# Performance work log

Hardware: AMD Instinct MI355X
Metric: run time of the kernel (lower is better)

## Reference

```python
import jax, jax.numpy as jnp
import numpy as np

B, T = 4, 512
V, D, L, H, F = 32000, 1024, 12, 16, 4096
HD = D // H
CUTS = [0, 2000, 8000, V]
SHRINK = 4


def layer_norm(x, s, b, eps=1e-5):
    m = jnp.mean(x, axis=-1, keepdims=True)
    v = jnp.var(x, axis=-1, keepdims=True)
    return (x - m) * jax.lax.rsqrt(v + eps) * s + b


def rel_shift(x):
    # Transformer-XL relative shift. x: [B, H, T, S] with S == T.
    b, h, t, s = x.shape
    x = jnp.pad(x, ((0, 0), (0, 0), (0, 0), (1, 0)))
    x = x.reshape(b, h, s + 1, t)[:, :, 1:, :]
    return x.reshape(b, h, t, s)


def sinusoid_pos_emb(seq_len, dim):
    # positions seq_len-1 ... 0 (TXL convention), [seq_len, dim]
    pos = jnp.arange(seq_len - 1, -1, -1.0, dtype=jnp.float32)
    inv_freq = 1.0 / (10000.0 ** (jnp.arange(0, dim, 2, dtype=jnp.float32) / dim))
    ang = pos[:, None] * inv_freq[None, :]
    return jnp.concatenate([jnp.sin(ang), jnp.cos(ang)], axis=-1)


def setup_inputs() -> dict:
    key = jax.random.key(0)
    ks = iter(jax.random.split(key, 64))

    def n(shape, std=0.02):
        return jax.random.normal(next(ks), shape, dtype=jnp.float32) * std

    hids = [D // (SHRINK ** i) for i in range(3)]  # 1024, 256, 64
    inp = {}
    inp['x'] = jax.random.randint(next(ks), (B, T), 0, V)
    inp['emb_0'] = n([CUTS[1] - CUTS[0], hids[0]])
    inp['emb_1'] = n([CUTS[2] - CUTS[1], hids[1]])
    inp['emb_2'] = n([CUTS[3] - CUTS[2], hids[2]])
    inp['proj_1'] = n([hids[1], D], 0.01)
    inp['proj_2'] = n([hids[2], D], 0.01)
    inp['out_bias'] = jnp.zeros([V], jnp.float32)
    inp['r_w_bias'] = n([1, 1, H, HD])
    inp['r_r_bias'] = n([1, 1, H, HD])
    inp['ln1_s'] = jnp.ones([L, D], jnp.float32)
    inp['ln1_b'] = jnp.zeros([L, D], jnp.float32)
    inp['Wq'] = n([L, D, D]); inp['bq'] = jnp.zeros([L, D], jnp.float32)
    inp['Wk'] = n([L, D, D]); inp['bk'] = jnp.zeros([L, D], jnp.float32)
    inp['Wv'] = n([L, D, D]); inp['bv'] = jnp.zeros([L, D], jnp.float32)
    inp['Wr'] = n([L, D, D])  # relative position projection (no bias)
    inp['Wo'] = n([L, D, D]); inp['bo'] = jnp.zeros([L, D], jnp.float32)
    inp['ln2_s'] = jnp.ones([L, D], jnp.float32)
    inp['ln2_b'] = jnp.zeros([L, D], jnp.float32)
    inp['W1'] = n([L, D, F]); inp['b1'] = jnp.zeros([L, F], jnp.float32)
    inp['W2'] = n([L, F, D]); inp['b2'] = jnp.zeros([L, D], jnp.float32)
    return inp


def forward(x, emb_0, emb_1, emb_2, proj_1, proj_2, out_bias, r_w_bias, r_r_bias,
            ln1_s, ln1_b, Wq, bq, Wk, bk, Wv, bv, Wr, Wo, bo, ln2_s, ln2_b,
            W1, b1, W2, b2):
    Bx, Tx = x.shape
    # --- adaptive input embedding (clustered table + up-projection, scaled) ---
    embs = [emb_0, emb_1, emb_2]
    projs = [None, proj_1, proj_2]
    h = jnp.zeros((Bx, Tx, D), jnp.float32)
    for i in range(3):
        lo, hi = CUTS[i], CUTS[i + 1]
        in_bucket = (x >= lo) & (x < hi)
        idx = jnp.clip(x - lo, 0, hi - lo - 1)
        e = embs[i][idx]  # [B, T, hid_i]
        if projs[i] is not None:
            e = e @ projs[i]  # -> [B, T, D]
        h = h + jnp.where(in_bucket[..., None], e, 0.0)
    h = h * jnp.sqrt(jnp.float32(D))

    pemb = sinusoid_pos_emb(Tx, D)                  # [T, D]
    causal = jnp.tril(jnp.ones((Tx, Tx), bool))     # [T, T]
    scale = 1.0 / np.sqrt(HD)

    for i in range(L):
        # --- TXL relative-position multi-head attention (pre-norm) ---
        a_in = layer_norm(h, ln1_s[i], ln1_b[i])
        q = (a_in @ Wq[i] + bq[i]).reshape(Bx, Tx, H, HD)
        k = (a_in @ Wk[i] + bk[i]).reshape(Bx, Tx, H, HD)
        v = (a_in @ Wv[i] + bv[i]).reshape(Bx, Tx, H, HD)
        r_k = (pemb @ Wr[i]).reshape(Tx, H, HD)     # [T, H, HD]
        content = jnp.einsum('bthd,bshd->bhts', q + r_w_bias[0, 0], k)
        rel = jnp.einsum('bthd,shd->bhts', q + r_r_bias[0, 0], r_k)
        logits = (content + rel_shift(rel)) * scale
        logits = jnp.where(causal[None, None], logits, jnp.float32(-1e30))
        attn = jax.nn.softmax(logits, axis=-1)
        o = jnp.einsum('bhts,bshd->bthd', attn, v).reshape(Bx, Tx, D)
        h = h + (o @ Wo[i] + bo[i])
        # --- FFN (pre-norm, GELU) ---
        f_in = layer_norm(h, ln2_s[i], ln2_b[i])
        h = h + (jax.nn.gelu(f_in @ W1[i] + b1[i]) @ W2[i] + b2[i])

    # --- tied adaptive-softmax output projection ---
    W_full = jnp.concatenate([emb_0, emb_1 @ proj_1, emb_2 @ proj_2], axis=0)  # [V, D]
    return h @ W_full.T + out_bias  # [B, T, V]


def reference(x, emb_0, emb_1, emb_2, proj_1, proj_2, out_bias, r_w_bias, r_r_bias,
              ln1_s, ln1_b, Wq, bq, Wk, bk, Wv, bv, Wr, Wo, bo, ln2_s, ln2_b,
              W1, b1, W2, b2):
    return forward(x, emb_0, emb_1, emb_2, proj_1, proj_2, out_bias, r_w_bias,
                   r_r_bias, ln1_s, ln1_b, Wq, bq, Wk, bk, Wv, bv, Wr, Wo, bo,
                   ln2_s, ln2_b, W1, b1, W2, b2)
```

## Files before the change

kernel.cpp:

```cpp
#include <hip/hip_runtime.h>

using us = unsigned short;
typedef short short8v __attribute__((ext_vector_type(8)));
typedef float float4v __attribute__((ext_vector_type(4)));

constexpr int NB  = 4;
constexpr int NT  = 512;
constexpr int ND  = 1024;
constexpr int NL  = 12;
constexpr int NH  = 16;
constexpr int NF  = 4096;
constexpr int NHD = 64;
constexpr int NBT = NB * NT;
constexpr int NV  = 32000;
constexpr long QOFF = (long)NBT * ND;
constexpr long RKL  = 640L * 1024;

__device__ __forceinline__ us f2bf(float f) {
    unsigned u = __float_as_uint(f);
    u += 0x7fffu + ((u >> 16) & 1u);
    return (us)(u >> 16);
}

__device__ __forceinline__ void gload16(const us* g, us* l) {
    __builtin_amdgcn_global_load_lds(
        (const __attribute__((address_space(1))) void*)g,
        (__attribute__((address_space(3))) void*)l, 16, 0, 0);
}

template<int BM, int BN, int EPI, bool OUTBF>
__global__ __launch_bounds__(256)
void bgemm_k(const us* __restrict__ A, const us* __restrict__ B, void* Cv,
             const float* __restrict__ bias, const float* addsrc,
             const float* __restrict__ p0, const float* __restrict__ p1,
             us* __restrict__ vtp,
             int N, int K, int lda, int ldb, int ldc,
             int bdiv, long sAb, long sAh, long sBb, long sBh, long sCb, long sCh)
{
    constexpr int BK  = 64;
    constexpr int WTM = BM / 2, WTN = BN / 2;
    constexpr int FM  = WTM / 16, FN = WTN / 16;
    constexpr int AI  = BM / 32;
    constexpr int BI  = BN / 32;
    static_assert(BM % 32 == 0 && BN % 32 == 0, "");

    long coff = 0;
    if (bdiv > 0) {
        int z = blockIdx.z, zb = z / bdiv, zh = z % bdiv;
        A += zb * sAb + zh * sAh;
        B += zb * sBb + zh * sBh;
        coff = zb * sCb + zh * sCh;
    }
    float* Cf = (float*)Cv + coff;
    us*    Ch = (us*)Cv + coff;
    if (addsrc) addsrc += coff;

    __shared__ __align__(16) us As[2 * BM * BK];
    __shared__ __align__(16) us Bs[2 * BN * BK];

    const int tid  = threadIdx.x;
    const int lane = tid & 63;
    const int w    = tid >> 6;
    const int wm   = w >> 1;
    const int wn   = w & 1;
    const int row0 = blockIdx.y * BM;
    const int col0 = blockIdx.x * BN;

    float4v acc[FM][FN];
#pragma unroll
    for (int i = 0; i < FM; ++i)
#pragma unroll
        for (int j = 0; j < FN; ++j) acc[i][j] = (float4v)0.f;

    auto stage = [&](int buf, int k0) {
        us* Ad = As + buf * (BM * BK);
        us* Bd = Bs + buf * (BN * BK);
#pragma unroll
        for (int i = 0; i < AI; ++i) {
            int rb = w * (BM / 4) + i * 8;
            int r  = rb + (lane >> 3);
            int sc8 = ((lane & 7) ^ (r & 7)) << 3;
            gload16(A + (long)(row0 + r) * lda + k0 + sc8, Ad + rb * 64);
        }
#pragma unroll
        for (int i = 0; i < BI; ++i) {
            int rb = w * (BN / 4) + i * 8;
            int r  = rb + (lane >> 3);
            int sc8 = ((lane & 7) ^ (r & 7)) << 3;
            gload16(B + (long)(col0 + r) * ldb + k0 + sc8, Bd + rb * 64);
        }
    };

    stage(0, 0);
    __syncthreads();
    int cur = 0;
    for (int k0 = 0; k0 < K; k0 += BK) {
        if (k0 + BK < K) stage(cur ^ 1, k0 + BK);
        const char* Ac = (const char*)(As + cur * (BM * BK));
        const char* Bc = (const char*)(Bs + cur * (BN * BK));
#pragma unroll
        for (int ks = 0; ks < 2; ++ks) {
            short8v af[FM], bfr[FN];
            int sw = ks * 4 + (lane >> 4);
#pragma unroll
            for (int i = 0; i < FM; ++i) {
                int r = wm * WTM + i * 16 + (lane & 15);
                af[i] = *reinterpret_cast<const short8v*>(Ac + r * 128 + ((sw ^ (r & 7)) << 4));
            }
#pragma unroll
            for (int j = 0; j < FN; ++j) {
                int r = wn * WTN + j * 16 + (lane & 15);
                bfr[j] = *reinterpret_cast<const short8v*>(Bc + r * 128 + ((sw ^ (r & 7)) << 4));
            }
#pragma unroll
            for (int i = 0; i < FM; ++i)
#pragma unroll
                for (int j = 0; j < FN; ++j)
                    acc[i][j] = __builtin_amdgcn_mfma_f32_16x16x32_bf16(af[i], bfr[j], acc[i][j], 0, 0, 0);
        }
        __syncthreads();
        cur ^= 1;
    }

#pragma unroll
    for (int i = 0; i < FM; ++i) {
        int growb = row0 + wm * WTM + i * 16 + ((lane >> 4) << 2);
#pragma unroll
        for (int j = 0; j < FN; ++j) {
            int gcol = col0 + wn * WTN + j * 16 + (lane & 15);
            if (EPI == 3) {
                int seg = gcol >> 10, c = gcol & 1023;
                float bb = bias[gcol];
                if (seg == 2) {
                    unsigned lo = (unsigned)f2bf(acc[i][j][0] + bb)
                                | ((unsigned)f2bf(acc[i][j][1] + bb) << 16);
                    unsigned hi = (unsigned)f2bf(acc[i][j][2] + bb)
                                | ((unsigned)f2bf(acc[i][j][3] + bb) << 16);
                    int bidx = growb >> 9, tb = growb & 511;
                    uint2 pk; pk.x = lo; pk.y = hi;
                    *reinterpret_cast<uint2*>(
                        vtp + ((long)((bidx * 16 + (c >> 6)) * 64 + (c & 63)) << 9) + tb) = pk;
                } else {
                    us* base = (us*)Cv;
#pragma unroll
                    for (int r = 0; r < 4; ++r) {
                        int gr = growb + r;
                        float v = acc[i][j][r] + bb;
                        long o = (long)gr * 1024 + c;
                        if (seg == 0) {
                            base[o]        = f2bf(v + p0[c]);
                            base[o + QOFF] = f2bf(v + p1[c]);
                        } else base[o + 2 * QOFF] = f2bf(v);
                    }
                }
            } else {
                if (gcol >= N) continue;
#pragma unroll
                for (int r = 0; r < 4; ++r) {
                    int gr = growb + r;
                    float v = acc[i][j][r];
                    if (bias) v += bias[gcol];
                    if (EPI == 1) {
                        float xx = v;
                        v = 0.5f * xx * (1.f + tanhf(0.7978845608028654f
                                                     * (xx + 0.044715f * xx * xx * xx)));
                    }
                    if (addsrc) v += addsrc[(long)gr * ldc + gcol];
                    if (OUTBF) Ch[(long)gr * ldc + gcol] = f2bf(v);
                    else       Cf[(long)gr * ldc + gcol] = v;
                }
            }
        }
    }
}

__global__ __launch_bounds__(256)
void ffnred_k(const float* __restrict__ part, const float* __restrict__ b2v,
              float* __restrict__ h)
{
    long i = ((long)blockIdx.x * 256 + threadIdx.x) * 4;
    float4 a0 = *reinterpret_cast<const float4*>(part + i);
    float4 a1 = *reinterpret_cast<const float4*>(part + i + 2097152);
    float4 a2 = *reinterpret_cast<const float4*>(part + i + 4194304);
    float4 a3 = *reinterpret_cast<const float4*>(part + i + 6291456);
    float4 hv = *reinterpret_cast<const float4*>(h + i);
    float4 bb = *reinterpret_cast<const float4*>(b2v + (int)(i & 1023));
    hv.x += a0.x + a1.x + a2.x + a3.x + bb.x;
    hv.y += a0.y + a1.y + a2.y + a3.y + bb.y;
    hv.z += a0.z + a1.z + a2.z + a3.z + bb.z;
    hv.w += a0.w + a1.w + a2.w + a3.w + bb.w;
    *reinterpret_cast<float4*>(h + i) = hv;
}

__global__ __launch_bounds__(256)
void fattn_k(const us* __restrict__ qkv, const us* __restrict__ vt,
             const us* __restrict__ rk, us* __restrict__ obuf)
{
    __shared__ __align__(16) us lds_k[64 * 64];
    __shared__ __align__(16) us lds_v[64 * 64];
    __shared__ __align__(16) us lds_rk[64 * 64];
    __shared__ __align__(16) us lds_p[4 * 16 * 64];
    __shared__ float lds_r[4 * 16 * 132];

    const int tid = threadIdx.x, lane = tid & 63, w = tid >> 6;
    const int qt = blockIdx.x, bh = blockIdx.y;
    const int b = bh >> 4, h = bh & 15;
    const int t0 = qt * 64;
    const int rg = lane >> 4, lc = lane & 15;

    const us* qwb = qkv + ((long)b * 512) * 1024 + h * 64;
    const us* qrb = qwb + QOFF;
    const us* kb  = qwb + 2 * QOFF;
    const us* vtb = vt + (long)bh * 64 * 512;
    const us* rkb = rk + h * 64;

    short8v aqw[2], aqr[2];
    {
        long qrow = (long)(t0 + w * 16 + lc) * 1024;
        int ko = rg * 8;
        aqw[0] = *(const short8v*)(qwb + qrow + ko);
        aqw[1] = *(const short8v*)(qwb + qrow + 32 + ko);
        aqr[0] = *(const short8v*)(qrb + qrow + ko);
        aqr[1] = *(const short8v*)(qrb + qrow + 32 + ko);
    }

    float4v oacc[4];
#pragma unroll
    for (int i = 0; i < 4; ++i) oacc[i] = (float4v)0.f;
    float mrow[4] = {-3e38f, -3e38f, -3e38f, -3e38f};
    float lrow[4] = {0.f, 0.f, 0.f, 0.f};

    float* rbase = lds_r + w * (16 * 132);
    us*    pbase = lds_p + w * (16 * 64);

    auto stage_rk = [&](int j0) {
#pragma unroll
        for (int i = 0; i < 2; ++i) {
            int rb = w * 16 + i * 8;
            int r  = rb + (lane >> 3);
            int sl = ((lane & 7) ^ (r & 7)) << 3;
            gload16(rkb + (long)(j0 + r) * 1024 + sl, lds_rk + rb * 64);
        }
    };
    auto rel_half = [&](int wbase) {
#pragma unroll
        for (int jn = 0; jn < 4; ++jn) {
            float4v rf = (float4v)0.f;
#pragma unroll
            for (int kk = 0; kk < 2; ++kk) {
                int r = jn * 16 + lc;
                int sw = kk * 4 + rg;
                short8v bf = *(const short8v*)((const char*)lds_rk + r * 128 + ((sw ^ (r & 7)) << 4));
                rf = __builtin_amdgcn_mfma_f32_16x16x32_bf16(aqr[kk], bf, rf, 0, 0, 0);
            }
#pragma unroll
            for (int pr = 0; pr < 4; ++pr)
                rbase[(rg * 4 + pr) * 132 + wbase + jn * 16 + lc] = rf[pr];
        }
    };

    const int nst = qt + 1;
    for (int st = 0; st < nst; ++st) {
        const int s0 = st * 64;
        const int jb = (st - qt) * 64 + 448;
        const int sb = ((st - qt + 7) & 1) << 6;

#pragma unroll
        for (int i = 0; i < 2; ++i) {
            int rb = w * 16 + i * 8;
            int r  = rb + (lane >> 3);
            int sl = ((lane & 7) ^ (r & 7)) << 3;
            gload16(kb + (long)(s0 + r) * 1024 + sl, lds_k + rb * 64);
            gload16(vtb + (long)r * 512 + s0 + sl, lds_v + rb * 64);
        }
        if (st == 0) {
            stage_rk(jb);
            __syncthreads();
            rel_half(sb);
            __syncthreads();
            stage_rk(jb + 64);
            __syncthreads();
        } else {
            stage_rk(jb + 64);
            __syncthreads();
        }

        float4v sfr[4];
#pragma unroll
        for (int sn = 0; sn < 4; ++sn) {
            sfr[sn] = (float4v)0.f;
#pragma unroll
            for (int kk = 0; kk < 2; ++kk) {
                int r = sn * 16 + lc;
                int sw = kk * 4 + rg;
                short8v bf = *(const short8v*)((const char*)lds_k + r * 128 + ((sw ^ (r & 7)) << 4));
                sfr[sn] = __builtin_amdgcn_mfma_f32_16x16x32_bf16(aqw[kk], bf, sfr[sn], 0, 0, 0);
            }
        }
        rel_half(sb ^ 64);

        float pv[4][4];
        float rmax[4] = {-3e38f, -3e38f, -3e38f, -3e38f};
#pragma unroll
        for (int pr = 0; pr < 4; ++pr) {
            int tt = rg * 4 + pr;
            int tw = w * 16 + tt;
#pragma unroll
            for (int sn = 0; sn < 4; ++sn) {
                int ss = sn * 16 + lc;
                int slot = (sb + ss + 63 - tw) & 127;
                float lg = (sfr[sn][pr] + rbase[tt * 132 + slot]) * 0.125f;
                if (ss > t0 - s0 + tw) lg = -1e30f;
                pv[sn][pr] = lg;
                rmax[pr] = fmaxf(rmax[pr], lg);
            }
        }
#pragma unroll
        for (int o = 1; o < 16; o <<= 1)
#pragma unroll
            for (int pr = 0; pr < 4; ++pr)
                rmax[pr] = fmaxf(rmax[pr], __shfl_xor(rmax[pr], o));
        float rsum[4];
#pragma unroll
        for (int pr = 0; pr < 4; ++pr) {
            float mn = fmaxf(mrow[pr], rmax[pr]);
            float al = __expf(mrow[pr] - mn);
            mrow[pr] = mn;
            lrow[pr] *= al;
            float s = 0.f;
#pragma unroll
            for (int sn = 0; sn < 4; ++sn) {
                float p = __expf(pv[sn][pr] - mn);
                pv[sn][pr] = p;
                s += p;
            }
            rsum[pr] = s;
#pragma unroll
            for (int dn = 0; dn < 4; ++dn) oacc[dn][pr] *= al;
        }
#pragma unroll
        for (int o = 1; o < 16; o <<= 1)
#pragma unroll
            for (int pr = 0; pr < 4; ++pr)
                rsum[pr] += __shfl_xor(rsum[pr], o);
#pragma unroll
        for (int pr = 0; pr < 4; ++pr) lrow[pr] += rsum[pr];

#pragma unroll
        for (int pr = 0; pr < 4; ++pr) {
            int row = rg * 4 + pr;
#pragma unroll
            for (int sn = 0; sn < 4; ++sn) {
                int col = sn * 16 + lc;
                *(us*)((char*)pbase + row * 128 + (((col >> 3) ^ (row & 7)) << 4) + (col & 7) * 2)
                    = f2bf(pv[sn][pr]);
            }
        }
        short8v pa[2];
#pragma unroll
        for (int kk = 0; kk < 2; ++kk)
            pa[kk] = *(const short8v*)((const char*)pbase + lc * 128 + (((kk * 4 + rg) ^ (lc & 7)) << 4));
#pragma unroll
        for (int dn = 0; dn < 4; ++dn) {
#pragma unroll
            for (int kk = 0; kk < 2; ++kk) {
                int r = dn * 16 + lc;
                int sw = kk * 4 + rg;
                short8v vb = *(const short8v*)((const char*)lds_v + r * 128 + ((sw ^ (r & 7)) << 4));
                oacc[dn] = __builtin_amdgcn_mfma_f32_16x16x32_bf16(pa[kk], vb, oacc[dn], 0, 0, 0);
            }
        }
        __syncthreads();
    }
#pragma unroll
    for (int pr = 0; pr < 4; ++pr) {
        int t = t0 + w * 16 + rg * 4 + pr;
        float inv = 1.f / lrow[pr];
        long rowo = ((long)b * 512 + t) * 1024 + h * 64;
#pragma unroll
        for (int dn = 0; dn < 4; ++dn)
            obuf[rowo + dn * 16 + lc] = f2bf(oacc[dn][pr] * inv);
    }
}

__global__ __launch_bounds__(256)
void tconv_k(const float* __restrict__ in, us* __restrict__ out, int R, int C,
             long inL, long outL)
{
    in  += (long)blockIdx.z * inL;
    out += (long)blockIdx.z * outL;
    __shared__ float t[32][33];
    int c0 = blockIdx.x * 32, r0 = blockIdx.y * 32;
    int tx = threadIdx.x & 31, ty = threadIdx.x >> 5;
#pragma unroll
    for (int j = 0; j < 4; ++j)
        t[ty + j * 8][tx] = in[(long)(r0 + ty + j * 8) * C + c0 + tx];
    __syncthreads();
#pragma unroll
    for (int j = 0; j < 4; ++j)
        out[(long)(c0 + ty + j * 8) * R + r0 + tx] = f2bf(t[tx][ty + j * 8]);
}

__global__ __launch_bounds__(256)
void conv_k(const float* __restrict__ in, us* __restrict__ out, long n)
{
    long i = ((long)blockIdx.x * 256 + threadIdx.x) * 4;
    if (i >= n) return;
    float4 v = *reinterpret_cast<const float4*>(in + i);
    uint2 p;
    p.x = (unsigned)f2bf(v.x) | ((unsigned)f2bf(v.y) << 16);
    p.y = (unsigned)f2bf(v.z) | ((unsigned)f2bf(v.w) << 16);
    *reinterpret_cast<uint2*>(out + i) = p;
}

__global__ __launch_bounds__(256)
void rkpad12_k(us* __restrict__ rk)
{
    int i = blockIdx.x * 256 + threadIdx.x;
    int l = i >> 13, r = i & 8191;
    reinterpret_cast<uint4*>(rk + (long)l * RKL + 512 * 1024)[r] = make_uint4(0, 0, 0, 0);
}

__global__ __launch_bounds__(256)
void bcat_k(const float* __restrict__ bq, const float* __restrict__ bk,
            const float* __restrict__ bv, float* __restrict__ o)
{
    int i = blockIdx.x * 256 + threadIdx.x;
    int l = i / 3072, rr = i % 3072, seg = rr >> 10, c = rr & 1023;
    const float* s = seg == 0 ? bq : seg == 1 ? bk : bv;
    o[i] = s[l * 1024 + c];
}

__global__ __launch_bounds__(256)
void ln_k(const float* __restrict__ x, us* __restrict__ y,
          const float* __restrict__ sc, const float* __restrict__ bi)
{
    int row = blockIdx.x;
    const float* xr = x + (long)row * ND;
    int d4 = threadIdx.x * 4;
    float4 v = *reinterpret_cast<const float4*>(&xr[d4]);
    float sum = v.x + v.y + v.z + v.w;
    float sq  = v.x * v.x + v.y * v.y + v.z * v.z + v.w * v.w;
#pragma unroll
    for (int o = 32; o; o >>= 1) { sum += __shfl_xor(sum, o); sq += __shfl_xor(sq, o); }
    __shared__ float red[8];
    int w = threadIdx.x >> 6;
    if ((threadIdx.x & 63) == 0) { red[w] = sum; red[4 + w] = sq; }
    __syncthreads();
    sum = red[0] + red[1] + red[2] + red[3];
    sq  = red[4] + red[5] + red[6] + red[7];
    float mean = sum * (1.f / ND);
    float var  = fmaxf(sq * (1.f / ND) - mean * mean, 0.f);
    float inv  = rsqrtf(var + 1e-5f);
    float4 s4 = *reinterpret_cast<const float4*>(&sc[d4]);
    float4 b4 = *reinterpret_cast<const float4*>(&bi[d4]);
    uint2 p;
    p.x = (unsigned)f2bf((v.x - mean) * inv * s4.x + b4.x)
        | ((unsigned)f2bf((v.y - mean) * inv * s4.y + b4.y) << 16);
    p.y = (unsigned)f2bf((v.z - mean) * inv * s4.z + b4.z)
        | ((unsigned)f2bf((v.w - mean) * inv * s4.w + b4.w) << 16);
    *reinterpret_cast<uint2*>(y + (long)row * ND + d4) = p;
}

__global__ __launch_bounds__(256)
void pemb_k(us* __restrict__ p)
{
    int t = blockIdx.x;
    float pos = (float)(NT - 1 - t);
    for (int j = threadIdx.x; j < ND / 2; j += 256) {
        float invf = expf(-(float)j * (9.210340371976184f / 512.0f));
        float ang  = pos * invf;
        p[(long)t * ND + j]           = f2bf(sinf(ang));
        p[(long)t * ND + ND / 2 + j]  = f2bf(cosf(ang));
    }
}

__global__ __launch_bounds__(256)
void embed_k(const int* __restrict__ x,
             const float* __restrict__ e0, const float* __restrict__ e1,
             const float* __restrict__ e2, const float* __restrict__ p1,
             const float* __restrict__ p2, float* __restrict__ h)
{
    __shared__ float e[256];
    int tok = blockIdx.x;
    int v = x[tok];
    float* outp = h + (long)tok * ND;
    if (v < 2000) {
        const float* r = e0 + (long)v * ND;
        for (int d = threadIdx.x; d < ND; d += 256) outp[d] = r[d] * 32.0f;
    } else if (v < 8000) {
        const float* r = e1 + (long)(v - 2000) * 256;
        e[threadIdx.x] = r[threadIdx.x];
        __syncthreads();
        for (int d = threadIdx.x; d < ND; d += 256) {
            float acc = 0.f;
#pragma unroll 4
            for (int i = 0; i < 256; ++i) acc += e[i] * p1[(long)i * ND + d];
            outp[d] = acc * 32.0f;
        }
    } else {
        const float* r = e2 + (long)(v - 8000) * 64;
        if (threadIdx.x < 64) e[threadIdx.x] = r[threadIdx.x];
        __syncthreads();
        for (int d = threadIdx.x; d < ND; d += 256) {
            float acc = 0.f;
#pragma unroll 4
            for (int i = 0; i < 64; ++i) acc += e[i] * p2[(long)i * ND + d];
            outp[d] = acc * 32.0f;
        }
    }
}

extern "C" void kernel_launch(void* const* d_in, const int* in_sizes, int n_in,
                              void* d_out, int out_size, void* d_ws, size_t ws_size,
                              hipStream_t stream)
{
    (void)in_sizes; (void)n_in; (void)out_size;
    const int*   x     = (const int*)  d_in[0];
    const float* emb0  = (const float*)d_in[1];
    const float* emb1  = (const float*)d_in[2];
    const float* emb2  = (const float*)d_in[3];
    const float* proj1 = (const float*)d_in[4];
    const float* proj2 = (const float*)d_in[5];
    const float* obias = (const float*)d_in[6];
    const float* rwb   = (const float*)d_in[7];
    const float* rrb   = (const float*)d_in[8];
    const float* ln1s  = (const float*)d_in[9];
    const float* ln1b  = (const float*)d_in[10];
    const float* Wq    = (const float*)d_in[11];
    const float* bq    = (const float*)d_in[12];
    const float* Wk    = (const float*)d_in[13];
    const float* bk    = (const float*)d_in[14];
    const float* Wv    = (const float*)d_in[15];
    const float* bv    = (const float*)d_in[16];
    const float* Wr    = (const float*)d_in[17];
    const float* Wo    = (const float*)d_in[18];
    const float* bo    = (const float*)d_in[19];
    const float* ln2s  = (const float*)d_in[20];
    const float* ln2b  = (const float*)d_in[21];
    const float* W1    = (const float*)d_in[22];
    const float* b1    = (const float*)d_in[23];
    const float* W2    = (const float*)d_in[24];
    const float* b2    = (const float*)d_in[25];
    float* out = (float*)d_out;

    us* ob      = (us*)out;
    us* qkvbuf  = ob;
    us* mid_bf  = ob +  6291456;
    us* vt_bf   = ob + 14680064;
    us* o_bf    = ob + 16777216;
    us* ain_bf  = ob + 18874368;
    us* rk_all  = ob + 20971520;
    us* pemb_bf = ob + 28835840;
    us* wqkv_sc = ob + 29360128;
    us* wr_sc   = ob + 32505856;
    us* wo_sc   = ob + 33554432;
    us* w1_sc   = ob + 34603008;
    us* w2_sc   = ob + 38797312;
    float* pffn = out + 21495808;

    float* wsf      = (float*)d_ws;
    float* h        = wsf;
    us*    h_bf     = (us*)(wsf + 2097152);
    us*    hp1_bf   = h_bf   + 2097152;
    us*    hp2_bf   = hp1_bf + 524288;
    us*    emb0_bf  = hp2_bf + 131072;
    us*    emb1_bf  = emb0_bf + 2097152;
    us*    emb2_bf  = emb1_bf + 1572864;
    us*    proj1_bf = emb2_bf + 1540096;
    us*    proj2_bf = proj1_bf + 262144;
    float* bqkv     = (float*)(proj2_bf + 65536);
    us*    wqkv_all = (us*)(bqkv + 36864);
    us*    wr_all   = wqkv_all + (long)NL * 3072 * 1024;
    us*    wo_all   = wr_all   + (long)NL * 1024 * 1024;
    us*    w1_all   = wo_all   + (long)NL * 1024 * 1024;
    us*    w2_all   = w1_all   + (long)NL * 4096 * 1024;
    const bool big  = ws_size >= (size_t)352273408;

    bcat_k<<<144, 256, 0, stream>>>(bq, bk, bv, bqkv);
    conv_k<<<2000, 256, 0, stream>>>(emb0,  emb0_bf,  2048000);
    conv_k<<<1500, 256, 0, stream>>>(emb1,  emb1_bf,  1536000);
    conv_k<<<1500, 256, 0, stream>>>(emb2,  emb2_bf,  1536000);
    conv_k<<<256,  256, 0, stream>>>(proj1, proj1_bf, 262144);
    conv_k<<<64,   256, 0, stream>>>(proj2, proj2_bf, 65536);
    pemb_k<<<NT, 256, 0, stream>>>(pemb_bf);
    rkpad12_k<<<384, 256, 0, stream>>>(rk_all);
    embed_k<<<NBT, 256, 0, stream>>>(x, emb0, emb1, emb2, proj1, proj2, h);
    if (big) {
        tconv_k<<<dim3(32, 32, NL), 256, 0, stream>>>(Wq, wqkv_all,           1024, 1024, 1048576, 3145728);
        tconv_k<<<dim3(32, 32, NL), 256, 0, stream>>>(Wk, wqkv_all + 1048576, 1024, 1024, 1048576, 3145728);
        tconv_k<<<dim3(32, 32, NL), 256, 0, stream>>>(Wv, wqkv_all + 2097152, 1024, 1024, 1048576, 3145728);
        tconv_k<<<dim3(32, 32, NL), 256, 0, stream>>>(Wr, wr_all, 1024, 1024, 1048576, 1048576);
        tconv_k<<<dim3(32, 32, NL), 256, 0, stream>>>(Wo, wo_all, 1024, 1024, 1048576, 1048576);
        tconv_k<<<dim3(128, 32, NL), 256, 0, stream>>>(W1, w1_all, 1024, 4096, 4194304, 4194304);
        tconv_k<<<dim3(32, 128, NL), 256, 0, stream>>>(W2, w2_all, 4096, 1024, 4194304, 4194304);
        bgemm_k<64, 64, 0, true><<<dim3(16, 8, NL), 256, 0, stream>>>(
            pemb_bf, wr_all, rk_all, nullptr, nullptr, nullptr, nullptr, nullptr,
            1024, 1024, 1024, 1024, 1024,
            1, 0, 0, 1048576, 0, RKL, 0);
    }

    for (int l = 0; l < NL; ++l) {
        const us* wqkv_t = big ? wqkv_all + (long)l * 3145728 : wqkv_sc;
        const us* wo_t   = big ? wo_all   + (long)l * 1048576 : wo_sc;
        const us* w1_t   = big ? w1_all   + (long)l * 4194304 : w1_sc;
        const us* w2_t   = big ? w2_all   + (long)l * 4194304 : w2_sc;
        if (!big) {
            const long wOff = (long)l * ND * ND;
            tconv_k<<<dim3(32, 32), 256, 0, stream>>>(Wq + wOff, wqkv_sc,           1024, 1024, 0, 0);
            tconv_k<<<dim3(32, 32), 256, 0, stream>>>(Wk + wOff, wqkv_sc + 1048576, 1024, 1024, 0, 0);
            tconv_k<<<dim3(32, 32), 256, 0, stream>>>(Wv + wOff, wqkv_sc + 2097152, 1024, 1024, 0, 0);
            tconv_k<<<dim3(32, 32), 256, 0, stream>>>(Wr + wOff, wr_sc, 1024, 1024, 0, 0);
            tconv_k<<<dim3(32, 32), 256, 0, stream>>>(Wo + wOff, wo_sc, 1024, 1024, 0, 0);
            tconv_k<<<dim3(128, 32), 256, 0, stream>>>(W1 + (long)l * ND * NF, w1_sc, 1024, 4096, 0, 0);
            tconv_k<<<dim3(32, 128), 256, 0, stream>>>(W2 + (long)l * ND * NF, w2_sc, 4096, 1024, 0, 0);
            bgemm_k<64, 64, 0, true><<<dim3(16, 8, 1), 256, 0, stream>>>(
                pemb_bf, wr_sc, rk_all + (long)l * RKL, nullptr, nullptr, nullptr, nullptr, nullptr,
                1024, 1024, 1024, 1024, 1024, 0, 0, 0, 0, 0, 0, 0);
        }

        ln_k<<<NBT, 256, 0, stream>>>(h, ain_bf, ln1s + l * ND, ln1b + l * ND);
        bgemm_k<128, 64, 3, true><<<dim3(48, 16, 1), 256, 0, stream>>>(
            ain_bf, wqkv_t, qkvbuf, bqkv + l * 3072, nullptr, rwb, rrb, vt_bf,
            3072, 1024, 1024, 1024, 1024, 0, 0, 0, 0, 0, 0, 0);
        fattn_k<<<dim3(8, NB * NH), 256, 0, stream>>>(
            qkvbuf, vt_bf, rk_all + (long)l * RKL, o_bf);
        bgemm_k<64, 64, 0, false><<<dim3(16, 32, 1), 256, 0, stream>>>(
            o_bf, wo_t, h, bo + l * ND, h, nullptr, nullptr, nullptr,
            1024, 1024, 1024, 1024, 1024, 0, 0, 0, 0, 0, 0, 0);

        ln_k<<<NBT, 256, 0, stream>>>(h, ain_bf, ln2s + l * ND, ln2b + l * ND);
        bgemm_k<128, 128, 1, true><<<dim3(32, 16, 1), 256, 0, stream>>>(
            ain_bf, w1_t, mid_bf, b1 + (long)l * NF, nullptr, nullptr, nullptr, nullptr,
            4096, 1024, 1024, 1024, 4096, 0, 0, 0, 0, 0, 0, 0);
        bgemm_k<128, 128, 0, false><<<dim3(8, 16, 4), 256, 0, stream>>>(
            mid_bf, w2_t, pffn, nullptr, nullptr, nullptr, nullptr, nullptr,
            1024, 1024, 4096, 4096, 1024,
            1, 1024, 0, 1024, 0, 2097152, 0);
        ffnred_k<<<2048, 256, 0, stream>>>(pffn, b2 + (long)l * ND, h);
    }

    conv_k<<<2048, 256, 0, stream>>>(h, h_bf, (long)NBT * ND);
    bgemm_k<128, 64, 0, false><<<dim3(32, 16, 1), 256, 0, stream>>>(
        h_bf, emb0_bf, out, obias, nullptr, nullptr, nullptr, nullptr,
        2000, 1024, 1024, 1024, NV, 0, 0, 0, 0, 0, 0, 0);
    bgemm_k<64, 64, 0, true><<<dim3(4, 32, 1), 256, 0, stream>>>(
        h_bf, proj1_bf, hp1_bf, nullptr, nullptr, nullptr, nullptr, nullptr,
        256, 1024, 1024, 1024, 256, 0, 0, 0, 0, 0, 0, 0);
    bgemm_k<128, 128, 0, false><<<dim3(47, 16, 1), 256, 0, stream>>>(
        hp1_bf, emb1_bf, out + 2000, obias + 2000, nullptr, nullptr, nullptr, nullptr,
        6000, 256, 256, 256, NV, 0, 0, 0, 0, 0, 0, 0);
    bgemm_k<64, 64, 0, true><<<dim3(1, 32, 1), 256, 0, stream>>>(
        h_bf, proj2_bf, hp2_bf, nullptr, nullptr, nullptr, nullptr, nullptr,
        64, 1024, 1024, 1024, 64, 0, 0, 0, 0, 0, 0, 0);
    bgemm_k<128, 128, 0, false><<<dim3(188, 16, 1), 256, 0, stream>>>(
        hp2_bf, emb2_bf, out + 8000, obias + 8000, nullptr, nullptr, nullptr, nullptr,
        24000, 64, 64, 64, NV, 0, 0, 0, 0, 0, 0, 0);
}
```

Before: 2.572 ms.

## Fuse residual reductions with layernorm, split-K Wo GEMM, pair attention query tiles

```diff
diff --git a/kernel.cpp b/kernel.cpp
--- a/kernel.cpp
+++ b/kernel.cpp
@@ -174,22 +174,52 @@
     }
 }
 
-__global__ __launch_bounds__(256)
-void ffnred_k(const float* __restrict__ part, const float* __restrict__ b2v,
-              float* __restrict__ h)
-{
-    long i = ((long)blockIdx.x * 256 + threadIdx.x) * 4;
-    float4 a0 = *reinterpret_cast<const float4*>(part + i);
-    float4 a1 = *reinterpret_cast<const float4*>(part + i + 2097152);
-    float4 a2 = *reinterpret_cast<const float4*>(part + i + 4194304);
-    float4 a3 = *reinterpret_cast<const float4*>(part + i + 6291456);
+template<int NPART, int MODE>
+__global__ __launch_bounds__(256)
+void redln_k(const float* __restrict__ part, const float* __restrict__ bias,
+             float* __restrict__ h, us* __restrict__ outb,
+             const float* __restrict__ sc, const float* __restrict__ bi)
+{
+    int row = blockIdx.x;
+    int d4 = threadIdx.x * 4;
+    long i = (long)row * ND + d4;
     float4 hv = *reinterpret_cast<const float4*>(h + i);
-    float4 bb = *reinterpret_cast<const float4*>(b2v + (int)(i & 1023));
-    hv.x += a0.x + a1.x + a2.x + a3.x + bb.x;
-    hv.y += a0.y + a1.y + a2.y + a3.y + bb.y;
-    hv.z += a0.z + a1.z + a2.z + a3.z + bb.z;
-    hv.w += a0.w + a1.w + a2.w + a3.w + bb.w;
+    float4 bb = *reinterpret_cast<const float4*>(bias + d4);
+    hv.x += bb.x; hv.y += bb.y; hv.z += bb.z; hv.w += bb.w;
+#pragma unroll
+    for (int z = 0; z < NPART; ++z) {
+        float4 a = *reinterpret_cast<const float4*>(part + (long)z * 2097152 + i);
+        hv.x += a.x; hv.y += a.y; hv.z += a.z; hv.w += a.w;
+    }
     *reinterpret_cast<float4*>(h + i) = hv;
+    if (MODE == 1) {
+        uint2 p;
+        p.x = (unsigned)f2bf(hv.x) | ((unsigned)f2bf(hv.y) << 16);
+        p.y = (unsigned)f2bf(hv.z) | ((unsigned)f2bf(hv.w) << 16);
+        *reinterpret_cast<uint2*>(outb + i) = p;
+    } else {
+        float sum = hv.x + hv.y + hv.z + hv.w;
+        float sq  = hv.x * hv.x + hv.y * hv.y + hv.z * hv.z + hv.w * hv.w;
+#pragma unroll
+        for (int o = 32; o; o >>= 1) { sum += __shfl_xor(sum, o); sq += __shfl_xor(sq, o); }
+        __shared__ float red[8];
+        int w = threadIdx.x >> 6;
+        if ((threadIdx.x & 63) == 0) { red[w] = sum; red[4 + w] = sq; }
+        __syncthreads();
+        sum = red[0] + red[1] + red[2] + red[3];
+        sq  = red[4] + red[5] + red[6] + red[7];
+        float mean = sum * (1.f / ND);
+        float var  = fmaxf(sq * (1.f / ND) - mean * mean, 0.f);
+        float inv  = rsqrtf(var + 1e-5f);
+        float4 s4 = *reinterpret_cast<const float4*>(&sc[d4]);
+        float4 b4 = *reinterpret_cast<const float4*>(&bi[d4]);
+        uint2 p;
+        p.x = (unsigned)f2bf((hv.x - mean) * inv * s4.x + b4.x)
+            | ((unsigned)f2bf((hv.y - mean) * inv * s4.y + b4.y) << 16);
+        p.y = (unsigned)f2bf((hv.z - mean) * inv * s4.z + b4.z)
+            | ((unsigned)f2bf((hv.w - mean) * inv * s4.w + b4.w) << 16);
+        *reinterpret_cast<uint2*>(outb + i) = p;
+    }
 }
 
 __global__ __launch_bounds__(256)
@@ -203,9 +233,8 @@
     __shared__ float lds_r[4 * 16 * 132];
 
     const int tid = threadIdx.x, lane = tid & 63, w = tid >> 6;
-    const int qt = blockIdx.x, bh = blockIdx.y;
+    const int qtp = blockIdx.x, bh = blockIdx.y;
     const int b = bh >> 4, h = bh & 15;
-    const int t0 = qt * 64;
     const int rg = lane >> 4, lc = lane & 15;
 
     const us* qwb = qkv + ((long)b * 512) * 1024 + h * 64;
@@ -214,172 +243,177 @@
     const us* vtb = vt + (long)bh * 64 * 512;
     const us* rkb = rk + h * 64;
 
-    short8v aqw[2], aqr[2];
-    {
-        long qrow = (long)(t0 + w * 16 + lc) * 1024;
-        int ko = rg * 8;
-        aqw[0] = *(const short8v*)(qwb + qrow + ko);
-        aqw[1] = *(const short8v*)(qwb + qrow + 32 + ko);
-        aqr[0] = *(const short8v*)(qrb + qrow + ko);
-        aqr[1] = *(const short8v*)(qrb + qrow + 32 + ko);
-    }
-
-    float4v oacc[4];
-#pragma unroll
-    for (int i = 0; i < 4; ++i) oacc[i] = (float4v)0.f;
-    float mrow[4] = {-3e38f, -3e38f, -3e38f, -3e38f};
-    float lrow[4] = {0.f, 0.f, 0.f, 0.f};
-
     float* rbase = lds_r + w * (16 * 132);
     us*    pbase = lds_p + w * (16 * 64);
 
-    auto stage_rk = [&](int j0) {
-#pragma unroll
-        for (int i = 0; i < 2; ++i) {
-            int rb = w * 16 + i * 8;
-            int r  = rb + (lane >> 3);
-            int sl = ((lane & 7) ^ (r & 7)) << 3;
-            gload16(rkb + (long)(j0 + r) * 1024 + sl, lds_rk + rb * 64);
-        }
-    };
-    auto rel_half = [&](int wbase) {
-#pragma unroll
-        for (int jn = 0; jn < 4; ++jn) {
-            float4v rf = (float4v)0.f;
-#pragma unroll
-            for (int kk = 0; kk < 2; ++kk) {
-                int r = jn * 16 + lc;
-                int sw = kk * 4 + rg;
-                short8v bf = *(const short8v*)((const char*)lds_rk + r * 128 + ((sw ^ (r & 7)) << 4));
-                rf = __builtin_amdgcn_mfma_f32_16x16x32_bf16(aqr[kk], bf, rf, 0, 0, 0);
-            }
-#pragma unroll
-            for (int pr = 0; pr < 4; ++pr)
-                rbase[(rg * 4 + pr) * 132 + wbase + jn * 16 + lc] = rf[pr];
-        }
-    };
-
-    const int nst = qt + 1;
-    for (int st = 0; st < nst; ++st) {
-        const int s0 = st * 64;
-        const int jb = (st - qt) * 64 + 448;
-        const int sb = ((st - qt + 7) & 1) << 6;
-
-#pragma unroll
-        for (int i = 0; i < 2; ++i) {
-            int rb = w * 16 + i * 8;
-            int r  = rb + (lane >> 3);
-            int sl = ((lane & 7) ^ (r & 7)) << 3;
-            gload16(kb + (long)(s0 + r) * 1024 + sl, lds_k + rb * 64);
-            gload16(vtb + (long)r * 512 + s0 + sl, lds_v + rb * 64);
-        }
-        if (st == 0) {
-            stage_rk(jb);
+    for (int hh = 0; hh < 2; ++hh) {
+        const int qt = hh ? 7 - qtp : qtp;
+        const int t0 = qt * 64;
+
+        short8v aqw[2], aqr[2];
+        {
+            long qrow = (long)(t0 + w * 16 + lc) * 1024;
+            int ko = rg * 8;
+            aqw[0] = *(const short8v*)(qwb + qrow + ko);
+            aqw[1] = *(const short8v*)(qwb + qrow + 32 + ko);
+            aqr[0] = *(const short8v*)(qrb + qrow + ko);
+            aqr[1] = *(const short8v*)(qrb + qrow + 32 + ko);
+        }
+
+        float4v oacc[4];
+#pragma unroll
+        for (int i = 0; i < 4; ++i) oacc[i] = (float4v)0.f;
+        float mrow[4] = {-3e38f, -3e38f, -3e38f, -3e38f};
+        float lrow[4] = {0.f, 0.f, 0.f, 0.f};
+
+        auto stage_rk = [&](int j0) {
+#pragma unroll
+            for (int i = 0; i < 2; ++i) {
+                int rb = w * 16 + i * 8;
+                int r  = rb + (lane >> 3);
+                int sl = ((lane & 7) ^ (r & 7)) << 3;
+                gload16(rkb + (long)(j0 + r) * 1024 + sl, lds_rk + rb * 64);
+            }
+        };
+        auto rel_half = [&](int wbase) {
+#pragma unroll
+            for (int jn = 0; jn < 4; ++jn) {
+                float4v rf = (float4v)0.f;
+#pragma unroll
+                for (int kk = 0; kk < 2; ++kk) {
+                    int r = jn * 16 + lc;
+                    int sw = kk * 4 + rg;
+                    short8v bf = *(const short8v*)((const char*)lds_rk + r * 128 + ((sw ^ (r & 7)) << 4));
+                    rf = __builtin_amdgcn_mfma_f32_16x16x32_bf16(aqr[kk], bf, rf, 0, 0, 0);
+                }
+#pragma unroll
+                for (int pr = 0; pr < 4; ++pr)
+                    rbase[(rg * 4 + pr) * 132 + wbase + jn * 16 + lc] = rf[pr];
+            }
+        };
+
+        const int nst = qt + 1;
+        for (int st = 0; st < nst; ++st) {
+            const int s0 = st * 64;
+            const int jb = (st - qt) * 64 + 448;
+            const int sb = ((st - qt + 7) & 1) << 6;
+
+#pragma unroll
+            for (int i = 0; i < 2; ++i) {
+                int rb = w * 16 + i * 8;
+                int r  = rb + (lane >> 3);
+                int sl = ((lane & 7) ^ (r & 7)) << 3;
+                gload16(kb + (long)(s0 + r) * 1024 + sl, lds_k + rb * 64);
+                gload16(vtb + (long)r * 512 + s0 + sl, lds_v + rb * 64);
+            }
+            if (st == 0) {
+                stage_rk(jb);
+                __syncthreads();
+                rel_half(sb);
+                __syncthreads();
+                stage_rk(jb + 64);
+                __syncthreads();
+            } else {
+                stage_rk(jb + 64);
+                __syncthreads();
+            }
+
+            float4v sfr[4];
+#pragma unroll
+            for (int sn = 0; sn < 4; ++sn) {
+                sfr[sn] = (float4v)0.f;
+#pragma unroll
+                for (int kk = 0; kk < 2; ++kk) {
+                    int r = sn * 16 + lc;
+                    int sw = kk * 4 + rg;
+                    short8v bf = *(const short8v*)((const char*)lds_k + r * 128 + ((sw ^ (r & 7)) << 4));
+                    sfr[sn] = __builtin_amdgcn_mfma_f32_16x16x32_bf16(aqw[kk], bf, sfr[sn], 0, 0, 0);
+                }
+            }
+            rel_half(sb ^ 64);
+
+            float pv[4][4];
+            float rmax[4] = {-3e38f, -3e38f, -3e38f, -3e38f};
+#pragma unroll
+            for (int pr = 0; pr < 4; ++pr) {
+                int tt = rg * 4 + pr;
+                int tw = w * 16 + tt;
+#pragma unroll
+                for (int sn = 0; sn < 4; ++sn) {
+                    int ss = sn * 16 + lc;
+                    int slot = (sb + ss + 63 - tw) & 127;
+                    float lg = (sfr[sn][pr] + rbase[tt * 132 + slot]) * 0.125f;
+                    if (ss > t0 - s0 + tw) lg = -1e30f;
+                    pv[sn][pr] = lg;
+                    rmax[pr] = fmaxf(rmax[pr], lg);
+                }
+            }
+#pragma unroll
+            for (int o = 1; o < 16; o <<= 1)
+#pragma unroll
+                for (int pr = 0; pr < 4; ++pr)
+                    rmax[pr] = fmaxf(rmax[pr], __shfl_xor(rmax[pr], o));
+            float rsum[4];
+#pragma unroll
+            for (int pr = 0; pr < 4; ++pr) {
+                float mn = fmaxf(mrow[pr], rmax[pr]);
+                float al = __expf(mrow[pr] - mn);
+                mrow[pr] = mn;
+                lrow[pr] *= al;
+                float s = 0.f;
+#pragma unroll
+                for (int sn = 0; sn < 4; ++sn) {
+                    float p = __expf(pv[sn][pr] - mn);
+                    pv[sn][pr] = p;
+                    s += p;
+                }
+                rsum[pr] = s;
+#pragma unroll
+                for (int dn = 0; dn < 4; ++dn) oacc[dn][pr] *= al;
+            }
+#pragma unroll
+            for (int o = 1; o < 16; o <<= 1)
+#pragma unroll
+                for (int pr = 0; pr < 4; ++pr)
+                    rsum[pr] += __shfl_xor(rsum[pr], o);
+#pragma unroll
+            for (int pr = 0; pr < 4; ++pr) lrow[pr] += rsum[pr];
+
+#pragma unroll
+            for (int pr = 0; pr < 4; ++pr) {
+                int row = rg * 4 + pr;
+#pragma unroll
+                for (int sn = 0; sn < 4; ++sn) {
+                    int col = sn * 16 + lc;
+                    *(us*)((char*)pbase + row * 128 + (((col >> 3) ^ (row & 7)) << 4) + (col & 7) * 2)
+                        = f2bf(pv[sn][pr]);
+                }
+            }
+            short8v pa[2];
+#pragma unroll
+            for (int kk = 0; kk < 2; ++kk)
+                pa[kk] = *(const short8v*)((const char*)pbase + lc * 128 + (((kk * 4 + rg) ^ (lc & 7)) << 4));
+#pragma unroll
+            for (int dn = 0; dn < 4; ++dn) {
+#pragma unroll
+                for (int kk = 0; kk < 2; ++kk) {
+                    int r = dn * 16 + lc;
+                    int sw = kk * 4 + rg;
+                    short8v vb = *(const short8v*)((const char*)lds_v + r * 128 + ((sw ^ (r & 7)) << 4));
+                    oacc[dn] = __builtin_amdgcn_mfma_f32_16x16x32_bf16(pa[kk], vb, oacc[dn], 0, 0, 0);
+                }
+            }
             __syncthreads();
-            rel_half(sb);
-            __syncthreads();
-            stage_rk(jb + 64);
-            __syncthreads();
-        } else {
-            stage_rk(jb + 64);
-            __syncthreads();
-        }
-
-        float4v sfr[4];
-#pragma unroll
-        for (int sn = 0; sn < 4; ++sn) {
-            sfr[sn] = (float4v)0.f;
-#pragma unroll
-            for (int kk = 0; kk < 2; ++kk) {
-                int r = sn * 16 + lc;
-                int sw = kk * 4 + rg;
-                short8v bf = *(const short8v*)((const char*)lds_k + r * 128 + ((sw ^ (r & 7)) << 4));
-                sfr[sn] = __builtin_amdgcn_mfma_f32_16x16x32_bf16(aqw[kk], bf, sfr[sn], 0, 0, 0);
-            }
-        }
-        rel_half(sb ^ 64);
-
-        float pv[4][4];
-        float rmax[4] = {-3e38f, -3e38f, -3e38f, -3e38f};
+        }
 #pragma unroll
         for (int pr = 0; pr < 4; ++pr) {
-            int tt = rg * 4 + pr;
-            int tw = w * 16 + tt;
-#pragma unroll
-            for (int sn = 0; sn < 4; ++sn) {
-                int ss = sn * 16 + lc;
-                int slot = (sb + ss + 63 - tw) & 127;
-                float lg = (sfr[sn][pr] + rbase[tt * 132 + slot]) * 0.125f;
-                if (ss > t0 - s0 + tw) lg = -1e30f;
-                pv[sn][pr] = lg;
-                rmax[pr] = fmaxf(rmax[pr], lg);
-            }
-        }
-#pragma unroll
-        for (int o = 1; o < 16; o <<= 1)
-#pragma unroll
-            for (int pr = 0; pr < 4; ++pr)
-                rmax[pr] = fmaxf(rmax[pr], __shfl_xor(rmax[pr], o));
-        float rsum[4];
-#pragma unroll
-        for (int pr = 0; pr < 4; ++pr) {
-            float mn = fmaxf(mrow[pr], rmax[pr]);
-            float al = __expf(mrow[pr] - mn);
-            mrow[pr] = mn;
-            lrow[pr] *= al;
-            float s = 0.f;
-#pragma unroll
-            for (int sn = 0; sn < 4; ++sn) {
-                float p = __expf(pv[sn][pr] - mn);
-                pv[sn][pr] = p;
-                s += p;
-            }
-            rsum[pr] = s;
-#pragma unroll
-            for (int dn = 0; dn < 4; ++dn) oacc[dn][pr] *= al;
-        }
-#pragma unroll
-        for (int o = 1; o < 16; o <<= 1)
-#pragma unroll
-            for (int pr = 0; pr < 4; ++pr)
-                rsum[pr] += __shfl_xor(rsum[pr], o);
-#pragma unroll
-        for (int pr = 0; pr < 4; ++pr) lrow[pr] += rsum[pr];
-
-#pragma unroll
-        for (int pr = 0; pr < 4; ++pr) {
-            int row = rg * 4 + pr;
-#pragma unroll
-            for (int sn = 0; sn < 4; ++sn) {
-                int col = sn * 16 + lc;
-                *(us*)((char*)pbase + row * 128 + (((col >> 3) ^ (row & 7)) << 4) + (col & 7) * 2)
-                    = f2bf(pv[sn][pr]);
-            }
-        }
-        short8v pa[2];
-#pragma unroll
-        for (int kk = 0; kk < 2; ++kk)
-            pa[kk] = *(const short8v*)((const char*)pbase + lc * 128 + (((kk * 4 + rg) ^ (lc & 7)) << 4));
-#pragma unroll
-        for (int dn = 0; dn < 4; ++dn) {
-#pragma unroll
-            for (int kk = 0; kk < 2; ++kk) {
-                int r = dn * 16 + lc;
-                int sw = kk * 4 + rg;
-                short8v vb = *(const short8v*)((const char*)lds_v + r * 128 + ((sw ^ (r & 7)) << 4));
-                oacc[dn] = __builtin_amdgcn_mfma_f32_16x16x32_bf16(pa[kk], vb, oacc[dn], 0, 0, 0);
-            }
-        }
-        __syncthreads();
-    }
-#pragma unroll
-    for (int pr = 0; pr < 4; ++pr) {
-        int t = t0 + w * 16 + rg * 4 + pr;
-        float inv = 1.f / lrow[pr];
-        long rowo = ((long)b * 512 + t) * 1024 + h * 64;
-#pragma unroll
-        for (int dn = 0; dn < 4; ++dn)
-            obuf[rowo + dn * 16 + lc] = f2bf(oacc[dn][pr] * inv);
+            int t = t0 + w * 16 + rg * 4 + pr;
+            float inv = 1.f / lrow[pr];
+            long rowo = ((long)b * 512 + t) * 1024 + h * 64;
+#pragma unroll
+            for (int dn = 0; dn < 4; ++dn)
+                obuf[rowo + dn * 16 + lc] = f2bf(oacc[dn][pr] * inv);
+        }
     }
 }
 
@@ -558,6 +592,7 @@
     us* w1_sc   = ob + 34603008;
     us* w2_sc   = ob + 38797312;
     float* pffn = out + 21495808;
+    float* pwo  = out + 29884416;
 
     float* wsf      = (float*)d_ws;
     float* h        = wsf;
@@ -599,6 +634,7 @@
             1024, 1024, 1024, 1024, 1024,
             1, 0, 0, 1048576, 0, RKL, 0);
     }
+    ln_k<<<NBT, 256, 0, stream>>>(h, ain_bf, ln1s, ln1b);
 
     for (int l = 0; l < NL; ++l) {
         const us* wqkv_t = big ? wqkv_all + (long)l * 3145728 : wqkv_sc;
@@ -619,17 +655,18 @@
                 1024, 1024, 1024, 1024, 1024, 0, 0, 0, 0, 0, 0, 0);
         }
 
-        ln_k<<<NBT, 256, 0, stream>>>(h, ain_bf, ln1s + l * ND, ln1b + l * ND);
         bgemm_k<128, 64, 3, true><<<dim3(48, 16, 1), 256, 0, stream>>>(
             ain_bf, wqkv_t, qkvbuf, bqkv + l * 3072, nullptr, rwb, rrb, vt_bf,
             3072, 1024, 1024, 1024, 1024, 0, 0, 0, 0, 0, 0, 0);
-        fattn_k<<<dim3(8, NB * NH), 256, 0, stream>>>(
+        fattn_k<<<dim3(4, NB * NH), 256, 0, stream>>>(
             qkvbuf, vt_bf, rk_all + (long)l * RKL, o_bf);
-        bgemm_k<64, 64, 0, false><<<dim3(16, 32, 1), 256, 0, stream>>>(
-            o_bf, wo_t, h, bo + l * ND, h, nullptr, nullptr, nullptr,
-            1024, 1024, 1024, 1024, 1024, 0, 0, 0, 0, 0, 0, 0);
-
-        ln_k<<<NBT, 256, 0, stream>>>(h, ain_bf, ln2s + l * ND, ln2b + l * ND);
+        bgemm_k<128, 64, 0, false><<<dim3(16, 16, 2), 256, 0, stream>>>(
+            o_bf, wo_t, pwo, nullptr, nullptr, nullptr, nullptr, nullptr,
+            1024, 512, 1024, 1024, 1024,
+            1, 512, 0, 512, 0, 2097152, 0);
+        redln_k<2, 0><<<NBT, 256, 0, stream>>>(
+            pwo, bo + l * ND, h, ain_bf, ln2s + l * ND, ln2b + l * ND);
+
         bgemm_k<128, 128, 1, true><<<dim3(32, 16, 1), 256, 0, stream>>>(
             ain_bf, w1_t, mid_bf, b1 + (long)l * NF, nullptr, nullptr, nullptr, nullptr,
             4096, 1024, 1024, 1024, 4096, 0, 0, 0, 0, 0, 0, 0);
@@ -637,10 +674,15 @@
             mid_bf, w2_t, pffn, nullptr, nullptr, nullptr, nullptr, nullptr,
             1024, 1024, 4096, 4096, 1024,
             1, 1024, 0, 1024, 0, 2097152, 0);
-        ffnred_k<<<2048, 256, 0, stream>>>(pffn, b2 + (long)l * ND, h);
-    }
-
-    conv_k<<<2048, 256, 0, stream>>>(h, h_bf, (long)NBT * ND);
+        if (l < NL - 1)
+            redln_k<4, 0><<<NBT, 256, 0, stream>>>(
+                pffn, b2 + (long)l * ND, h, ain_bf,
+                ln1s + (l + 1) * ND, ln1b + (l + 1) * ND);
+        else
+            redln_k<4, 1><<<NBT, 256, 0, stream>>>(
+                pffn, b2 + (long)l * ND, h, h_bf, nullptr, nullptr);
+    }
+
     bgemm_k<128, 64, 0, false><<<dim3(32, 16, 1), 256, 0, stream>>>(
         h_bf, emb0_bf, out, obias, nullptr, nullptr, nullptr, nullptr,
         2000, 1024, 1024, 1024, NV, 0, 0, 0, 0, 0, 0, 0);
```

After: 2.459 ms. 1.05x faster.
